# Performance work log

Hardware: AMD Instinct MI355X
Metric: run time of the kernel (lower is better)

The kernel has to match this reference:

```python
import jax, jax.numpy as jnp
import numpy as np

B, T, L, D = 512, 100, 256, 128
DEPTH = 8                 # perfect binary tree depth -> path length DEPTH+1
P = DEPTH + 1
N_PER_TREE = 2 * L - 1    # 511 nodes per tree (heap layout)
N_TOTAL = T * N_PER_TREE  # 51100 global nodes


def _build_paths():
    # Heap layout per tree: internal nodes 0..L-2, leaves L-1..2L-2.
    # Path for leaf l = chain of heap ancestors from root to leaf.
    local = np.zeros((L, P), dtype=np.int32)
    for l in range(L):
        node = L - 1 + l
        chain = []
        while True:
            chain.append(node)
            if node == 0:
                break
            node = (node - 1) // 2
        local[l] = np.array(chain[::-1], dtype=np.int32)
    offs = (np.arange(T, dtype=np.int32) * N_PER_TREE)[:, None, None]
    return local[None, :, :] + offs  # [T, L, P] global node ids


def setup_inputs() -> dict:
    key = jax.random.key(0)
    k1, k2, k3, k4, k5, k6 = jax.random.split(key, 6)
    paths = jnp.asarray(_build_paths())
    # GBDT multi-hot: exactly one activated leaf per tree per sample
    leaf = jax.random.randint(k1, (B, T), 0, L)
    cross = (jnp.zeros((B, T, L), jnp.float32)
             .at[jnp.arange(B)[:, None], jnp.arange(T)[None, :], leaf]
             .set(1.0)
             .reshape(B, T * L))
    s = 1.0 / float(np.sqrt(D))  # torch LSTM init range
    node_emb = jax.random.normal(k2, (N_TOTAL, D), jnp.float32) * 0.01
    w_ih = jax.random.uniform(k3, (4 * D, D), jnp.float32, -s, s)
    w_hh = jax.random.uniform(k4, (4 * D, D), jnp.float32, -s, s)
    b_ih = jax.random.uniform(k5, (4 * D,), jnp.float32, -s, s)
    b_hh = jax.random.uniform(k6, (4 * D,), jnp.float32, -s, s)
    return {"cross_features": cross, "node_emb": node_emb, "w_ih": w_ih,
            "w_hh": w_hh, "b_ih": b_ih, "b_hh": b_hh, "paths": paths}


def _lstm_last_h(x, w_ih, w_hh, b_ih, b_hh):
    # x: [S, P, D] -> final hidden state [S, D]; torch gate order i, f, g, o
    S = x.shape[0]
    d = w_hh.shape[1]
    bias = b_ih + b_hh

    def step(carry, x_t):
        h, c = carry
        g = x_t @ w_ih.T + h @ w_hh.T + bias          # [S, 4D]
        i, f, gg, o = jnp.split(g, 4, axis=-1)
        c = jax.nn.sigmoid(f) * c + jax.nn.sigmoid(i) * jnp.tanh(gg)
        h = jax.nn.sigmoid(o) * jnp.tanh(c)
        return (h, c), None

    h0 = jnp.zeros((S, d), x.dtype)
    (h, _), _ = jax.lax.scan(step, (h0, h0), jnp.swapaxes(x, 0, 1))
    return h


def reference(cross_features, node_emb, w_ih, w_hh, b_ih, b_hh, paths):
    t, l, p = paths.shape
    b = cross_features.shape[0]
    d = node_emb.shape[1]
    cf = cross_features.reshape(b, t, l)
    leaf = jnp.argmax(cf, axis=-1)                    # [B, T] activated leaf per tree
    active = jnp.any(cf > 0, axis=-1)                 # [B, T] tree has an activated leaf
    node_ids = paths[jnp.arange(t)[None, :], leaf]    # [B, T, P] root-to-leaf global ids
    x = node_emb[node_ids].reshape(b * t, p, d)       # batched path gather
    h = _lstm_last_h(x, w_ih, w_hh, b_ih, b_hh).reshape(b, t, d)
    return jnp.where(active[..., None], h, jnp.zeros((), h.dtype))
```

## Files before the change

kernel.cpp:

```cpp
#include <hip/hip_runtime.h>
#include <math.h>


#define B_N 512
#define T_N 100
#define L_N 256
#define D_N 128
#define NPT 511

typedef __attribute__((ext_vector_type(8))) short short8;
typedef __attribute__((ext_vector_type(4))) float f32x4;
typedef __attribute__((ext_vector_type(4))) unsigned short ushort4v;

__device__ __forceinline__ unsigned short f2bf(float f) {
    unsigned u = __float_as_uint(f);
    return (unsigned short)((u + 0x7FFFu + ((u >> 16) & 1u)) >> 16);
}
__device__ __forceinline__ float bf2f(unsigned short b) {
    return __uint_as_float(((unsigned)b) << 16);
}
__device__ __forceinline__ float fsigmoid(float x) {
    return __builtin_amdgcn_rcpf(1.f + __builtin_amdgcn_exp2f(-1.44269504f * x));
}
__device__ __forceinline__ float ftanh(float x) {
    return 1.f - 2.f * __builtin_amdgcn_rcpf(1.f + __builtin_amdgcn_exp2f(2.88539009f * x));
}

__global__ __launch_bounds__(256) void pack_kernel(const float* __restrict__ w_ih,
                                                   const float* __restrict__ w_hh,
                                                   const float* __restrict__ b_ih,
                                                   const float* __restrict__ b_hh,
                                                   unsigned short* __restrict__ Bhi,
                                                   unsigned short* __restrict__ Blo,
                                                   float* __restrict__ bias) {
    const int idx = blockIdx.x * 256 + threadIdx.x;
    const int k  = idx & 255;
    const int np = idx >> 8;
    const float val = (k < 128) ? w_ih[(size_t)np * 128 + k]
                                : w_hh[(size_t)np * 128 + (k - 128)];
    const unsigned short hi = f2bf(val);
    const int kb = k >> 5, krel = k & 31, quad = krel >> 3, e = krel & 7;
    const int tn = np >> 4, col = np & 15, lane = quad * 16 + col;
    Bhi[(((size_t)kb * 32 + tn) * 64 + lane) * 8 + e] = hi;
    if (kb >= 4) {
        const unsigned short lo = f2bf(val - bf2f(hi));
        Blo[((((size_t)kb - 4) * 32 + tn) * 64 + lane) * 8 + e] = lo;
    }
    if (k == 0) bias[np] = b_ih[np] + b_hh[np];
}

__global__ __launch_bounds__(512, 2) void subtree_small_kernel(
    const float* __restrict__ node_emb,
    const unsigned short* __restrict__ Bhi,
    const unsigned short* __restrict__ Blo,
    const float* __restrict__ bias,
    float* __restrict__ h6, float* __restrict__ c6)
{
    __shared__ float hbuf[2][16][132];
    __shared__ float cbuf[2][16][132];
    __shared__ unsigned short AhiF[8 * 512];
    __shared__ unsigned short AloF[4 * 512];

    const int t    = blockIdx.x >> 2;
    const int s    = blockIdx.x & 3;
    const int tid  = threadIdx.x;
    const int idx  = tid >> 6;
    const int lane = tid & 63;
    const int ml   = lane & 15;
    const int quad = lane >> 4;
    const int j    = idx * 16 + ml;

    const float bi = bias[j];
    const float bf = bias[128 + j];
    const float bg = bias[256 + j];
    const float bo = bias[384 + j];

    const short8* Bh8 = reinterpret_cast<const short8*>(Bhi);
    const short8* Bl8 = reinterpret_cast<const short8*>(Blo);
    const short8* Ah8 = reinterpret_cast<const short8*>(AhiF);
    const short8* Al8 = reinterpret_cast<const short8*>(AloF);

    short8 bhR[8][4], blR[4][4];
    #pragma unroll
    for (int kb = 0; kb < 8; ++kb)
        #pragma unroll
        for (int g = 0; g < 4; ++g)
            bhR[kb][g] = Bh8[(kb * 32 + g * 8 + idx) * 64 + lane];
    #pragma unroll
    for (int kb = 0; kb < 4; ++kb)
        #pragma unroll
        for (int g = 0; g < 4; ++g)
            blR[kb][g] = Bl8[(kb * 32 + g * 8 + idx) * 64 + lane];

    for (int d = 0; d <= 6; ++d) {
        const int Mrows = (d == 0) ? 1 : (d == 1) ? 2 : (1 << (d - 2));
        const int pbase = (d >= 2) ? (s << (d - 2)) : 0;
        const bool root = (d == 0);
        const int cur = d & 1, prv = cur ^ 1;

        #pragma unroll
        for (int h2 = 0; h2 < 2; ++h2) {
            const int r  = tid & 15;
            const int k4 = (tid >> 4) + h2 * 32;
            const int k  = k4 * 4;
            int p = r; if (p > Mrows - 1) p = Mrows - 1;
            float4 v;
            if (k < 128) {
                const int local = (1 << d) - 1 + pbase + p;
                v = *reinterpret_cast<const float4*>(
                        node_emb + (size_t)(t * NPT + local) * D_N + k);
            } else if (root) {
                v = make_float4(0.f, 0.f, 0.f, 0.f);
            } else {
                const int pr = (d == 2) ? (s >> 1) : (p >> 1);
                v = *reinterpret_cast<const float4*>(&hbuf[prv][pr][k - 128]);
            }
            const int kb = k >> 5, qk = (k & 31) >> 3, e0 = k & 4;
            const ushort4v hv = { f2bf(v.x), f2bf(v.y), f2bf(v.z), f2bf(v.w) };
            *reinterpret_cast<ushort4v*>(&AhiF[(kb * 64 + qk * 16 + r) * 8 + e0]) = hv;
            if (k >= 128) {
                const ushort4v lv = { f2bf(v.x - bf2f(hv.x)), f2bf(v.y - bf2f(hv.y)),
                                      f2bf(v.z - bf2f(hv.z)), f2bf(v.w - bf2f(hv.w)) };
                *reinterpret_cast<ushort4v*>(
                    &AloF[((kb - 4) * 64 + qk * 16 + r) * 8 + e0]) = lv;
            }
        }
        __syncthreads();

        float cpre[4];
        #pragma unroll
        for (int rr = 0; rr < 4; ++rr) {
            int m = quad * 4 + rr;
            if (m > Mrows - 1) m = Mrows - 1;
            const int pr = (d == 2) ? (s >> 1) : (m >> 1);
            cpre[rr] = root ? 0.f : cbuf[prv][pr][j];
        }

        f32x4 acc[4];
        #pragma unroll
        for (int g = 0; g < 4; ++g) acc[g] = (f32x4)0.f;

        #pragma unroll
        for (int kb = 0; kb < 8; ++kb) {
            const short8 ah = Ah8[kb * 64 + lane];
            short8 al;
            if (kb >= 4) al = Al8[(kb - 4) * 64 + lane];
            #pragma unroll
            for (int g = 0; g < 4; ++g) {
                acc[g] = __builtin_amdgcn_mfma_f32_16x16x32_bf16(
                    ah, bhR[kb][g], acc[g], 0, 0, 0);
                if (kb >= 4) {
                    acc[g] = __builtin_amdgcn_mfma_f32_16x16x32_bf16(
                        ah, blR[kb - 4][g], acc[g], 0, 0, 0);
                    acc[g] = __builtin_amdgcn_mfma_f32_16x16x32_bf16(
                        al, bhR[kb][g], acc[g], 0, 0, 0);
                }
            }
        }

        #pragma unroll
        for (int rr = 0; rr < 4; ++rr) {
            const int m = quad * 4 + rr;
            if (m < Mrows) {
                const float ig = fsigmoid(acc[0][rr] + bi);
                const float fg = fsigmoid(acc[1][rr] + bf);
                const float gv = ftanh(acc[2][rr] + bg);
                const float og = fsigmoid(acc[3][rr] + bo);
                const float cn = fg * cpre[rr] + ig * gv;
                const float hn = og * ftanh(cn);
                hbuf[cur][m][j] = hn;
                cbuf[cur][m][j] = cn;
                if (d == 6) {
                    const size_t row = (size_t)(t * 64 + s * 16 + m) * D_N + j;
                    h6[row] = hn;
                    c6[row] = cn;
                }
            }
        }
        __syncthreads();
    }
}

template<int MT>
__global__ __launch_bounds__(512, 2) void mfma_level_kernel(
    const float* __restrict__ node_emb,
    const unsigned short* __restrict__ Bhi,
    const unsigned short* __restrict__ Blo,
    const float* __restrict__ bias,
    const float* __restrict__ h_prev,
    const float* __restrict__ c_prev,
    float* __restrict__ h_cur,
    float* __restrict__ c_cur,
    const int d, const int M, const int store_c)
{
    constexpr int NB = MT * 16;
    __shared__ unsigned short AhiF[8 * MT * 512];
    __shared__ unsigned short AloF[4 * MT * 512];

    const int tid = threadIdx.x;
    const int m0  = blockIdx.x * NB;

    {
        constexpr int tpr = 512 / NB;
        constexpr int nf  = 256 / tpr;
        const int r = tid / tpr;
        const int q = tid % tpr;
        int gm = m0 + r;
        if (gm > M - 1) gm = M - 1;
        const int mt = r >> 4, mlr = r & 15;
        const int t     = gm >> d;
        const int p     = gm - (t << d);
        const int local = (1 << d) - 1 + p;
        const float* xrow = node_emb + (size_t)(t * NPT + local) * D_N;
        const float* hrow = h_prev + (size_t)(gm >> 1) * D_N;
        #pragma unroll
        for (int i = 0; i < nf / 4; ++i) {
            const int k  = q * nf + i * 4;
            const int kb = k >> 5;
            const int qk = (k & 31) >> 3;
            const int e0 = k & 4;
            const float4 v = (k < 128)
                ? reinterpret_cast<const float4*>(xrow)[k >> 2]
                : reinterpret_cast<const float4*>(hrow)[(k - 128) >> 2];
            const ushort4v hv = { f2bf(v.x), f2bf(v.y), f2bf(v.z), f2bf(v.w) };
            *reinterpret_cast<ushort4v*>(
                &AhiF[((kb * MT + mt) * 64 + qk * 16 + mlr) * 8 + e0]) = hv;
            if (k >= 128) {
                const ushort4v lv = { f2bf(v.x - bf2f(hv.x)), f2bf(v.y - bf2f(hv.y)),
                                      f2bf(v.z - bf2f(hv.z)), f2bf(v.w - bf2f(hv.w)) };
                *reinterpret_cast<ushort4v*>(
                    &AloF[(((kb - 4) * MT + mt) * 64 + qk * 16 + mlr) * 8 + e0]) = lv;
            }
        }
    }
    __syncthreads();

    const int idx  = tid >> 6;
    const int lane = tid & 63;
    const int ml   = lane & 15;
    const int quad = lane >> 4;
    const int j    = idx * 16 + ml;

    float cpre[MT][4];
    #pragma unroll
    for (int mt = 0; mt < MT; ++mt)
        #pragma unroll
        for (int r = 0; r < 4; ++r) {
            int m = m0 + mt * 16 + quad * 4 + r;
            if (m > M - 1) m = M - 1;
            cpre[mt][r] = c_prev[(size_t)(m >> 1) * D_N + j];
        }

    f32x4 acc[MT][4];
    #pragma unroll
    for (int mt = 0; mt < MT; ++mt)
        #pragma unroll
        for (int g = 0; g < 4; ++g) acc[mt][g] = (f32x4)0.f;

    const short8* Bh8 = reinterpret_cast<const short8*>(Bhi);
    const short8* Bl8 = reinterpret_cast<const short8*>(Blo);
    const short8* Ah8 = reinterpret_cast<const short8*>(AhiF);
    const short8* Al8 = reinterpret_cast<const short8*>(AloF);

    short8 bh[4], bl[4];
    #pragma unroll
    for (int g = 0; g < 4; ++g)
        bh[g] = Bh8[(0 * 32 + g * 8 + idx) * 64 + lane];

    #pragma unroll
    for (int kb = 0; kb < 8; ++kb) {
        short8 bhn[4], bln[4];
        if (kb < 7) {
            #pragma unroll
            for (int g = 0; g < 4; ++g)
                bhn[g] = Bh8[((kb + 1) * 32 + g * 8 + idx) * 64 + lane];
            if (kb + 1 >= 4) {
                #pragma unroll
                for (int g = 0; g < 4; ++g)
                    bln[g] = Bl8[((kb + 1 - 4) * 32 + g * 8 + idx) * 64 + lane];
            }
        }
        short8 ah[MT], al[MT];
        #pragma unroll
        for (int mt = 0; mt < MT; ++mt)
            ah[mt] = Ah8[(kb * MT + mt) * 64 + lane];
        if (kb >= 4) {
            #pragma unroll
            for (int mt = 0; mt < MT; ++mt)
                al[mt] = Al8[((kb - 4) * MT + mt) * 64 + lane];
        }
        #pragma unroll
        for (int g = 0; g < 4; ++g) {
            #pragma unroll
            for (int mt = 0; mt < MT; ++mt) {
                acc[mt][g] = __builtin_amdgcn_mfma_f32_16x16x32_bf16(
                    ah[mt], bh[g], acc[mt][g], 0, 0, 0);
                if (kb >= 4) {
                    acc[mt][g] = __builtin_amdgcn_mfma_f32_16x16x32_bf16(
                        ah[mt], bl[g], acc[mt][g], 0, 0, 0);
                    acc[mt][g] = __builtin_amdgcn_mfma_f32_16x16x32_bf16(
                        al[mt], bh[g], acc[mt][g], 0, 0, 0);
                }
            }
        }
        if (kb < 7) {
            #pragma unroll
            for (int g = 0; g < 4; ++g) {
                bh[g] = bhn[g];
                if (kb + 1 >= 4) bl[g] = bln[g];
            }
        }
    }

    const float bi = bias[j];
    const float bf = bias[128 + j];
    const float bg = bias[256 + j];
    const float bo = bias[384 + j];
    #pragma unroll
    for (int mt = 0; mt < MT; ++mt) {
        #pragma unroll
        for (int r = 0; r < 4; ++r) {
            const int m = m0 + mt * 16 + quad * 4 + r;
            if (m < M) {
                const float ig = fsigmoid(acc[mt][0][r] + bi);
                const float fg = fsigmoid(acc[mt][1][r] + bf);
                const float gv = ftanh(acc[mt][2][r] + bg);
                const float og = fsigmoid(acc[mt][3][r] + bo);
                const float cn = fg * cpre[mt][r] + ig * gv;
                const float hn = og * ftanh(cn);
                if (store_c) c_cur[(size_t)m * D_N + j] = cn;
                h_cur[(size_t)m * D_N + j] = hn;
            }
        }
    }
}

__global__ __launch_bounds__(256) void gather_kernel(const float* __restrict__ cross,
                                                     const float* __restrict__ h8,
                                                     float* __restrict__ out) {
    const int bt   = blockIdx.x * 4 + (threadIdx.x >> 6);
    const int lane = threadIdx.x & 63;
    const int t    = bt % T_N;
    const float4 v = reinterpret_cast<const float4*>(cross + (size_t)bt * L_N)[lane];
    int idx = -1;
    if      (v.x > 0.f) idx = lane * 4 + 0;
    else if (v.y > 0.f) idx = lane * 4 + 1;
    else if (v.z > 0.f) idx = lane * 4 + 2;
    else if (v.w > 0.f) idx = lane * 4 + 3;
    const unsigned long long m = __ballot(idx >= 0);
    int lf = -1;
    if (m != 0ULL) {
        const int first = __builtin_ctzll(m);
        lf = __shfl(idx, first);
    }
    float2 o = make_float2(0.f, 0.f);
    if (lf >= 0)
        o = reinterpret_cast<const float2*>(h8 + (size_t)(t * L_N + lf) * D_N)[lane];
    reinterpret_cast<float2*>(out + (size_t)bt * D_N)[lane] = o;
}

extern "C" void kernel_launch(void* const* d_in, const int* in_sizes, int n_in,
                              void* d_out, int out_size, void* d_ws, size_t ws_size,
                              hipStream_t stream) {
    const float* cross    = (const float*)d_in[0];
    const float* node_emb = (const float*)d_in[1];
    const float* w_ih     = (const float*)d_in[2];
    const float* w_hh     = (const float*)d_in[3];
    const float* b_ih     = (const float*)d_in[4];
    const float* b_hh     = (const float*)d_in[5];
    float* out = (float*)d_out;
    float* ws  = (float*)d_ws;

    const size_t SA = (size_t)25600 * D_N;
    const size_t SB = (size_t)12800 * D_N;
    float* hA = ws;
    float* cA = hA + SA;
    float* hB = cA + SA;
    float* cB = hB + SB;
    float* bias = cB + SB;
    unsigned short* Bhi = (unsigned short*)(bias + 512);
    unsigned short* Blo = Bhi + 131072;

    pack_kernel<<<512, 256, 0, stream>>>(w_ih, w_hh, b_ih, b_hh, Bhi, Blo, bias);

    subtree_small_kernel<<<4 * T_N, 512, 0, stream>>>(node_emb, Bhi, Blo, bias,
                                                      hA, cA);

    {
        const int M7 = T_N << 7;
        mfma_level_kernel<2><<<M7 / 32, 512, 0, stream>>>(node_emb, Bhi, Blo, bias,
                                                          hA, cA, hB, cB, 7, M7, 1);
        const int M8 = T_N << 8;
        mfma_level_kernel<2><<<M8 / 32, 512, 0, stream>>>(node_emb, Bhi, Blo, bias,
                                                          hB, cB, hA, cA, 8, M8, 0);
    }
    gather_kernel<<<(B_N * T_N) / 4, 256, 0, stream>>>(cross, hA, out);
}
```

Before: 200.9 us.

## Fuse tree levels 7 and 8 into the per-subtree kernel

Folds the two separate per-level MFMA kernels into the subtree kernel, so each block goes on to compute levels 7 and 8 for its quarter-subtree. Weights stay resident in registers across all levels, and two kernel launches plus their inter-kernel gaps go away. Level-7 state still goes through global memory (h7g/c7g), which the same block reads back after a barrier. In exchange, levels 7 and 8 now run on only 400 blocks instead of many more, which lowers parallelism in the widest levels.

```diff
diff --git a/kernel.cpp b/kernel.cpp
--- a/kernel.cpp
+++ b/kernel.cpp
@@ -49,17 +49,18 @@
     if (k == 0) bias[np] = b_ih[np] + b_hh[np];
 }
 
-__global__ __launch_bounds__(512, 2) void subtree_small_kernel(
+__global__ __launch_bounds__(512, 2) void tree_kernel(
     const float* __restrict__ node_emb,
     const unsigned short* __restrict__ Bhi,
     const unsigned short* __restrict__ Blo,
     const float* __restrict__ bias,
-    float* __restrict__ h6, float* __restrict__ c6)
+    float* __restrict__ h7g, float* __restrict__ c7g,
+    float* __restrict__ h8)
 {
     __shared__ float hbuf[2][16][132];
     __shared__ float cbuf[2][16][132];
-    __shared__ unsigned short AhiF[8 * 512];
-    __shared__ unsigned short AloF[4 * 512];
+    __shared__ unsigned short AhiF[8 * 2 * 512];
+    __shared__ unsigned short AloF[4 * 2 * 512];
 
     const int t    = blockIdx.x >> 2;
     const int s    = blockIdx.x & 3;
@@ -117,12 +118,13 @@
             }
             const int kb = k >> 5, qk = (k & 31) >> 3, e0 = k & 4;
             const ushort4v hv = { f2bf(v.x), f2bf(v.y), f2bf(v.z), f2bf(v.w) };
-            *reinterpret_cast<ushort4v*>(&AhiF[(kb * 64 + qk * 16 + r) * 8 + e0]) = hv;
+            *reinterpret_cast<ushort4v*>(
+                &AhiF[((kb * 2 + 0) * 64 + qk * 16 + r) * 8 + e0]) = hv;
             if (k >= 128) {
                 const ushort4v lv = { f2bf(v.x - bf2f(hv.x)), f2bf(v.y - bf2f(hv.y)),
                                       f2bf(v.z - bf2f(hv.z)), f2bf(v.w - bf2f(hv.w)) };
                 *reinterpret_cast<ushort4v*>(
-                    &AloF[((kb - 4) * 64 + qk * 16 + r) * 8 + e0]) = lv;
+                    &AloF[(((kb - 4) * 2 + 0) * 64 + qk * 16 + r) * 8 + e0]) = lv;
             }
         }
         __syncthreads();
@@ -142,9 +144,9 @@
 
         #pragma unroll
         for (int kb = 0; kb < 8; ++kb) {
-            const short8 ah = Ah8[kb * 64 + lane];
+            const short8 ah = Ah8[(kb * 2 + 0) * 64 + lane];
             short8 al;
-            if (kb >= 4) al = Al8[(kb - 4) * 64 + lane];
+            if (kb >= 4) al = Al8[((kb - 4) * 2 + 0) * 64 + lane];
             #pragma unroll
             for (int g = 0; g < 4; ++g) {
                 acc[g] = __builtin_amdgcn_mfma_f32_16x16x32_bf16(
@@ -170,168 +172,155 @@
                 const float hn = og * ftanh(cn);
                 hbuf[cur][m][j] = hn;
                 cbuf[cur][m][j] = cn;
-                if (d == 6) {
-                    const size_t row = (size_t)(t * 64 + s * 16 + m) * D_N + j;
-                    h6[row] = hn;
-                    c6[row] = cn;
-                }
-            }
-        }
-        __syncthreads();
-    }
-}
-
-template<int MT>
-__global__ __launch_bounds__(512, 2) void mfma_level_kernel(
-    const float* __restrict__ node_emb,
-    const unsigned short* __restrict__ Bhi,
-    const unsigned short* __restrict__ Blo,
-    const float* __restrict__ bias,
-    const float* __restrict__ h_prev,
-    const float* __restrict__ c_prev,
-    float* __restrict__ h_cur,
-    float* __restrict__ c_cur,
-    const int d, const int M, const int store_c)
-{
-    constexpr int NB = MT * 16;
-    __shared__ unsigned short AhiF[8 * MT * 512];
-    __shared__ unsigned short AloF[4 * MT * 512];
-
-    const int tid = threadIdx.x;
-    const int m0  = blockIdx.x * NB;
+            }
+        }
+        __syncthreads();
+    }
 
     {
-        constexpr int tpr = 512 / NB;
-        constexpr int nf  = 256 / tpr;
-        const int r = tid / tpr;
-        const int q = tid % tpr;
-        int gm = m0 + r;
-        if (gm > M - 1) gm = M - 1;
-        const int mt = r >> 4, mlr = r & 15;
-        const int t     = gm >> d;
-        const int p     = gm - (t << d);
-        const int local = (1 << d) - 1 + p;
-        const float* xrow = node_emb + (size_t)(t * NPT + local) * D_N;
-        const float* hrow = h_prev + (size_t)(gm >> 1) * D_N;
-        #pragma unroll
-        for (int i = 0; i < nf / 4; ++i) {
-            const int k  = q * nf + i * 4;
-            const int kb = k >> 5;
-            const int qk = (k & 31) >> 3;
-            const int e0 = k & 4;
-            const float4 v = (k < 128)
-                ? reinterpret_cast<const float4*>(xrow)[k >> 2]
-                : reinterpret_cast<const float4*>(hrow)[(k - 128) >> 2];
+        #pragma unroll
+        for (int h2 = 0; h2 < 4; ++h2) {
+            const int r  = tid & 31;
+            const int k4 = (tid >> 5) + h2 * 16;
+            const int k  = k4 * 4;
+            const int mt = r >> 4, mlr = r & 15;
+            float4 v;
+            if (k < 128) {
+                const int local = 127 + s * 32 + r;
+                v = *reinterpret_cast<const float4*>(
+                        node_emb + (size_t)(t * NPT + local) * D_N + k);
+            } else {
+                v = *reinterpret_cast<const float4*>(&hbuf[0][r >> 1][k - 128]);
+            }
+            const int kb = k >> 5, qk = (k & 31) >> 3, e0 = k & 4;
             const ushort4v hv = { f2bf(v.x), f2bf(v.y), f2bf(v.z), f2bf(v.w) };
             *reinterpret_cast<ushort4v*>(
-                &AhiF[((kb * MT + mt) * 64 + qk * 16 + mlr) * 8 + e0]) = hv;
+                &AhiF[((kb * 2 + mt) * 64 + qk * 16 + mlr) * 8 + e0]) = hv;
             if (k >= 128) {
                 const ushort4v lv = { f2bf(v.x - bf2f(hv.x)), f2bf(v.y - bf2f(hv.y)),
                                       f2bf(v.z - bf2f(hv.z)), f2bf(v.w - bf2f(hv.w)) };
                 *reinterpret_cast<ushort4v*>(
-                    &AloF[(((kb - 4) * MT + mt) * 64 + qk * 16 + mlr) * 8 + e0]) = lv;
-            }
-        }
-    }
-    __syncthreads();
-
-    const int idx  = tid >> 6;
-    const int lane = tid & 63;
-    const int ml   = lane & 15;
-    const int quad = lane >> 4;
-    const int j    = idx * 16 + ml;
-
-    float cpre[MT][4];
-    #pragma unroll
-    for (int mt = 0; mt < MT; ++mt)
-        #pragma unroll
-        for (int r = 0; r < 4; ++r) {
-            int m = m0 + mt * 16 + quad * 4 + r;
-            if (m > M - 1) m = M - 1;
-            cpre[mt][r] = c_prev[(size_t)(m >> 1) * D_N + j];
-        }
-
-    f32x4 acc[MT][4];
-    #pragma unroll
-    for (int mt = 0; mt < MT; ++mt)
-        #pragma unroll
-        for (int g = 0; g < 4; ++g) acc[mt][g] = (f32x4)0.f;
-
-    const short8* Bh8 = reinterpret_cast<const short8*>(Bhi);
-    const short8* Bl8 = reinterpret_cast<const short8*>(Blo);
-    const short8* Ah8 = reinterpret_cast<const short8*>(AhiF);
-    const short8* Al8 = reinterpret_cast<const short8*>(AloF);
-
-    short8 bh[4], bl[4];
-    #pragma unroll
-    for (int g = 0; g < 4; ++g)
-        bh[g] = Bh8[(0 * 32 + g * 8 + idx) * 64 + lane];
-
-    #pragma unroll
-    for (int kb = 0; kb < 8; ++kb) {
-        short8 bhn[4], bln[4];
-        if (kb < 7) {
-            #pragma unroll
-            for (int g = 0; g < 4; ++g)
-                bhn[g] = Bh8[((kb + 1) * 32 + g * 8 + idx) * 64 + lane];
-            if (kb + 1 >= 4) {
+                    &AloF[(((kb - 4) * 2 + mt) * 64 + qk * 16 + mlr) * 8 + e0]) = lv;
+            }
+        }
+        __syncthreads();
+
+        #pragma unroll
+        for (int mt = 0; mt < 2; ++mt) {
+            float cpre[4];
+            #pragma unroll
+            for (int rr = 0; rr < 4; ++rr) {
+                const int m = mt * 16 + quad * 4 + rr;
+                cpre[rr] = cbuf[0][m >> 1][j];
+            }
+            f32x4 acc[4];
+            #pragma unroll
+            for (int g = 0; g < 4; ++g) acc[g] = (f32x4)0.f;
+            #pragma unroll
+            for (int kb = 0; kb < 8; ++kb) {
+                const short8 ah = Ah8[(kb * 2 + mt) * 64 + lane];
+                short8 al;
+                if (kb >= 4) al = Al8[((kb - 4) * 2 + mt) * 64 + lane];
                 #pragma unroll
-                for (int g = 0; g < 4; ++g)
-                    bln[g] = Bl8[((kb + 1 - 4) * 32 + g * 8 + idx) * 64 + lane];
-            }
-        }
-        short8 ah[MT], al[MT];
-        #pragma unroll
-        for (int mt = 0; mt < MT; ++mt)
-            ah[mt] = Ah8[(kb * MT + mt) * 64 + lane];
-        if (kb >= 4) {
-            #pragma unroll
-            for (int mt = 0; mt < MT; ++mt)
-                al[mt] = Al8[((kb - 4) * MT + mt) * 64 + lane];
-        }
-        #pragma unroll
-        for (int g = 0; g < 4; ++g) {
-            #pragma unroll
-            for (int mt = 0; mt < MT; ++mt) {
-                acc[mt][g] = __builtin_amdgcn_mfma_f32_16x16x32_bf16(
-                    ah[mt], bh[g], acc[mt][g], 0, 0, 0);
-                if (kb >= 4) {
-                    acc[mt][g] = __builtin_amdgcn_mfma_f32_16x16x32_bf16(
-                        ah[mt], bl[g], acc[mt][g], 0, 0, 0);
-                    acc[mt][g] = __builtin_amdgcn_mfma_f32_16x16x32_bf16(
-                        al[mt], bh[g], acc[mt][g], 0, 0, 0);
+                for (int g = 0; g < 4; ++g) {
+                    acc[g] = __builtin_amdgcn_mfma_f32_16x16x32_bf16(
+                        ah, bhR[kb][g], acc[g], 0, 0, 0);
+                    if (kb >= 4) {
+                        acc[g] = __builtin_amdgcn_mfma_f32_16x16x32_bf16(
+                            ah, blR[kb - 4][g], acc[g], 0, 0, 0);
+                        acc[g] = __builtin_amdgcn_mfma_f32_16x16x32_bf16(
+                            al, bhR[kb][g], acc[g], 0, 0, 0);
+                    }
                 }
             }
-        }
-        if (kb < 7) {
-            #pragma unroll
-            for (int g = 0; g < 4; ++g) {
-                bh[g] = bhn[g];
-                if (kb + 1 >= 4) bl[g] = bln[g];
-            }
-        }
-    }
-
-    const float bi = bias[j];
-    const float bf = bias[128 + j];
-    const float bg = bias[256 + j];
-    const float bo = bias[384 + j];
-    #pragma unroll
-    for (int mt = 0; mt < MT; ++mt) {
-        #pragma unroll
-        for (int r = 0; r < 4; ++r) {
-            const int m = m0 + mt * 16 + quad * 4 + r;
-            if (m < M) {
-                const float ig = fsigmoid(acc[mt][0][r] + bi);
-                const float fg = fsigmoid(acc[mt][1][r] + bf);
-                const float gv = ftanh(acc[mt][2][r] + bg);
-                const float og = fsigmoid(acc[mt][3][r] + bo);
-                const float cn = fg * cpre[mt][r] + ig * gv;
+            #pragma unroll
+            for (int rr = 0; rr < 4; ++rr) {
+                const int m = mt * 16 + quad * 4 + rr;
+                const float ig = fsigmoid(acc[0][rr] + bi);
+                const float fg = fsigmoid(acc[1][rr] + bf);
+                const float gv = ftanh(acc[2][rr] + bg);
+                const float og = fsigmoid(acc[3][rr] + bo);
+                const float cn = fg * cpre[rr] + ig * gv;
                 const float hn = og * ftanh(cn);
-                if (store_c) c_cur[(size_t)m * D_N + j] = cn;
-                h_cur[(size_t)m * D_N + j] = hn;
-            }
-        }
+                const size_t row = (size_t)(blockIdx.x * 32 + m) * D_N + j;
+                h7g[row] = hn;
+                c7g[row] = cn;
+            }
+        }
+        __syncthreads();
+    }
+
+    for (int pp = 0; pp < 2; ++pp) {
+        #pragma unroll
+        for (int h2 = 0; h2 < 4; ++h2) {
+            const int r  = tid & 31;
+            const int m2 = pp * 32 + r;
+            const int k4 = (tid >> 5) + h2 * 16;
+            const int k  = k4 * 4;
+            const int mt = r >> 4, mlr = r & 15;
+            float4 v;
+            if (k < 128) {
+                const int local = 255 + s * 64 + m2;
+                v = *reinterpret_cast<const float4*>(
+                        node_emb + (size_t)(t * NPT + local) * D_N + k);
+            } else {
+                v = *reinterpret_cast<const float4*>(
+                        h7g + (size_t)(blockIdx.x * 32 + (m2 >> 1)) * D_N + (k - 128));
+            }
+            const int kb = k >> 5, qk = (k & 31) >> 3, e0 = k & 4;
+            const ushort4v hv = { f2bf(v.x), f2bf(v.y), f2bf(v.z), f2bf(v.w) };
+            *reinterpret_cast<ushort4v*>(
+                &AhiF[((kb * 2 + mt) * 64 + qk * 16 + mlr) * 8 + e0]) = hv;
+            if (k >= 128) {
+                const ushort4v lv = { f2bf(v.x - bf2f(hv.x)), f2bf(v.y - bf2f(hv.y)),
+                                      f2bf(v.z - bf2f(hv.z)), f2bf(v.w - bf2f(hv.w)) };
+                *reinterpret_cast<ushort4v*>(
+                    &AloF[(((kb - 4) * 2 + mt) * 64 + qk * 16 + mlr) * 8 + e0]) = lv;
+            }
+        }
+        __syncthreads();
+
+        #pragma unroll
+        for (int mt = 0; mt < 2; ++mt) {
+            float cpre[4];
+            #pragma unroll
+            for (int rr = 0; rr < 4; ++rr) {
+                const int m2 = pp * 32 + mt * 16 + quad * 4 + rr;
+                cpre[rr] = c7g[(size_t)(blockIdx.x * 32 + (m2 >> 1)) * D_N + j];
+            }
+            f32x4 acc[4];
+            #pragma unroll
+            for (int g = 0; g < 4; ++g) acc[g] = (f32x4)0.f;
+            #pragma unroll
+            for (int kb = 0; kb < 8; ++kb) {
+                const short8 ah = Ah8[(kb * 2 + mt) * 64 + lane];
+                short8 al;
+                if (kb >= 4) al = Al8[((kb - 4) * 2 + mt) * 64 + lane];
+                #pragma unroll
+                for (int g = 0; g < 4; ++g) {
+                    acc[g] = __builtin_amdgcn_mfma_f32_16x16x32_bf16(
+                        ah, bhR[kb][g], acc[g], 0, 0, 0);
+                    if (kb >= 4) {
+                        acc[g] = __builtin_amdgcn_mfma_f32_16x16x32_bf16(
+                            ah, blR[kb - 4][g], acc[g], 0, 0, 0);
+                        acc[g] = __builtin_amdgcn_mfma_f32_16x16x32_bf16(
+                            al, bhR[kb][g], acc[g], 0, 0, 0);
+                    }
+                }
+            }
+            #pragma unroll
+            for (int rr = 0; rr < 4; ++rr) {
+                const int m2 = pp * 32 + mt * 16 + quad * 4 + rr;
+                const float ig = fsigmoid(acc[0][rr] + bi);
+                const float fg = fsigmoid(acc[1][rr] + bf);
+                const float gv = ftanh(acc[2][rr] + bg);
+                const float og = fsigmoid(acc[3][rr] + bo);
+                const float cn = fg * cpre[rr] + ig * gv;
+                const float hn = og * ftanh(cn);
+                h8[(size_t)((t << 8) + s * 64 + m2) * D_N + j] = hn;
+            }
+        }
+        __syncthreads();
     }
 }
 
@@ -371,28 +360,17 @@
     float* out = (float*)d_out;
     float* ws  = (float*)d_ws;
 
-    const size_t SA = (size_t)25600 * D_N;
-    const size_t SB = (size_t)12800 * D_N;
-    float* hA = ws;
-    float* cA = hA + SA;
-    float* hB = cA + SA;
-    float* cB = hB + SB;
-    float* bias = cB + SB;
+    float* h8   = ws;
+    float* h7g  = h8 + (size_t)25600 * D_N;
+    float* c7g  = h7g + (size_t)12800 * D_N;
+    float* bias = c7g + (size_t)12800 * D_N;
     unsigned short* Bhi = (unsigned short*)(bias + 512);
     unsigned short* Blo = Bhi + 131072;
 
     pack_kernel<<<512, 256, 0, stream>>>(w_ih, w_hh, b_ih, b_hh, Bhi, Blo, bias);
 
-    subtree_small_kernel<<<4 * T_N, 512, 0, stream>>>(node_emb, Bhi, Blo, bias,
-                                                      hA, cA);
-
-    {
-        const int M7 = T_N << 7;
-        mfma_level_kernel<2><<<M7 / 32, 512, 0, stream>>>(node_emb, Bhi, Blo, bias,
-                                                          hA, cA, hB, cB, 7, M7, 1);
-        const int M8 = T_N << 8;
-        mfma_level_kernel<2><<<M8 / 32, 512, 0, stream>>>(node_emb, Bhi, Blo, bias,
-                                                          hB, cB, hA, cA, 8, M8, 0);
-    }
-    gather_kernel<<<(B_N * T_N) / 4, 256, 0, stream>>>(cross, hA, out);
-}
+    tree_kernel<<<4 * T_N, 512, 0, stream>>>(node_emb, Bhi, Blo, bias,
+                                             h7g, c7g, h8);
+
+    gather_kernel<<<(B_N * T_N) / 4, 256, 0, stream>>>(cross, h8, out);
+}
```

Result: faster. 191.2 us (-4.9%).
